# Kernel optimization log

Hardware: AMD Instinct MI355X
Metric: run time of the kernel (lower is better)

## Reference

```python
import jax, jax.numpy as jnp
import numpy as np
from jax import lax

DIM = 1024      # model dim
DS = 16         # d_state
DC = 4          # d_conv
EXP = 2
DI = DIM * EXP  # d_inner = 2048
B, L = 2, 1024


def setup_inputs() -> dict:
    key = jax.random.key(0)
    ks = jax.random.split(key, 10)
    s = lambda k, shape, sc: jax.random.normal(k, shape, jnp.float32) * sc
    return {
        "x": s(ks[0], (B, L, DIM), 1.0),
        "norm_w": jnp.ones((DIM,), jnp.float32),
        "norm_b": jnp.zeros((DIM,), jnp.float32),
        "in_proj_w": s(ks[1], (2 * DI, DIM), DIM ** -0.5),
        "conv_w": s(ks[2], (DI, 1, DC), DC ** -0.5),   # depthwise: (out=DI, in/groups=1, K)
        "conv_b": jnp.zeros((DI,), jnp.float32),
        "x_proj_w": s(ks[3], (2 * DS + 1, DI), DI ** -0.5),
        "dt_w": s(ks[4], (DI, 1), 1.0),
        "dt_b": jax.random.uniform(ks[5], (DI,), jnp.float32, -0.001, 0.001),
        "A_log": s(ks[6], (DI, DS), 1.0),              # self.A (randn); A = -exp(A_log)
        "D_skip": jnp.ones((DI,), jnp.float32),
        "out_proj_w": s(ks[7], (DIM, DI), DI ** -0.5),
    }


def _ssm(x, x_proj_w, dt_w, dt_b, A_log, D_skip):
    # x: (B, L, DI)
    xp = jnp.einsum('bli,pi->blp', x, x_proj_w)            # (B, L, 2*DS+1)
    delta = jax.nn.softplus(xp[..., :1] * dt_w[:, 0] + dt_b)  # (B, L, DI)
    Bp = xp[..., 1:DS + 1]                                  # (B, L, DS)
    Cp = xp[..., DS + 1:]                                   # (B, L, DS)
    A = -jnp.exp(A_log)                                     # (DI, DS)
    dA = jnp.exp(delta[..., None] * A)                      # (B, L, DI, DS)
    dB = delta[..., None] * Bp[:, :, None, :] * x[..., None]  # (B, L, DI, DS)

    def step(h, inp):
        dA_t, dB_t, C_t = inp                               # (B,DI,DS),(B,DI,DS),(B,DS)
        h = dA_t * h + dB_t
        return h, jnp.einsum('bdn,bn->bd', h, C_t)

    h0 = jnp.zeros((x.shape[0], DI, DS), x.dtype)
    _, ys = lax.scan(step, h0, (jnp.swapaxes(dA, 0, 1),
                                jnp.swapaxes(dB, 0, 1),
                                jnp.swapaxes(Cp, 0, 1)))
    y = jnp.swapaxes(ys, 0, 1)                              # (B, L, DI)
    return y + x * D_skip


def reference(x, norm_w, norm_b, in_proj_w, conv_w, conv_b,
              x_proj_w, dt_w, dt_b, A_log, D_skip, out_proj_w):
    # LayerNorm
    mu = x.mean(-1, keepdims=True)
    var = ((x - mu) ** 2).mean(-1, keepdims=True)
    xn = (x - mu) * lax.rsqrt(var + 1e-5) * norm_w + norm_b
    # input projection and gate split
    xz = jnp.einsum('bld,pd->blp', xn, in_proj_w)           # (B, L, 2*DI)
    xi, z = xz[..., :DI], xz[..., DI:]
    # causal depthwise conv (torch pads K-1 both sides then slices [:L] == left-pad K-1)
    xc = lax.conv_general_dilated(jnp.swapaxes(xi, 1, 2), conv_w, (1,),
                                  [(DC - 1, 0)], feature_group_count=DI,
                                  dimension_numbers=('NCH', 'OIH', 'NCH'))
    xc = jnp.swapaxes(xc + conv_b[None, :, None], 1, 2)     # (B, L, DI)
    xc = jax.nn.silu(xc)
    y = _ssm(xc, x_proj_w, dt_w, dt_b, A_log, D_skip)
    y = y * jax.nn.silu(z)
    return x + jnp.einsum('bli,di->bld', y, out_proj_w)
```

## Files before the change

kernel.cpp:

```cpp
#include <hip/hip_runtime.h>
#include <stdint.h>

#define BATCH 2
#define SEQ   1024
#define DIM_  1024
#define DS_   16
#define DI_   2048
#define NTOK  (BATCH*SEQ)
#define NSEG  32
#define LSEG  (SEQ/NSEG)

typedef unsigned short u16;
using s16x8 = __attribute__((ext_vector_type(8))) short;
using f32x4 = __attribute__((ext_vector_type(4))) float;
using u16x4 = __attribute__((ext_vector_type(4))) unsigned short;
using u16x8 = __attribute__((ext_vector_type(8))) unsigned short;

__device__ __forceinline__ float bf2f(u16 u) {
  union { unsigned int i; float f; } c; c.i = ((unsigned int)u) << 16; return c.f;
}
__device__ __forceinline__ u16 f2bf(float f) {
  union { float f; unsigned int i; } c; c.f = f;
  unsigned int r = c.i + 0x7fffu + ((c.i >> 16) & 1u);
  return (u16)(r >> 16);
}
__device__ __forceinline__ float softplus_f(float x) {
  return (x > 15.f) ? x : __logf(1.f + __expf(x));
}

__global__ __launch_bounds__(256) void cvt_kernel(const float* __restrict__ a,
    u16* __restrict__ o, int n4) {
  int i = blockIdx.x * 256 + threadIdx.x;
  if (i >= n4) return;
  float4 v = ((const float4*)a)[i];
  u16x4 r; r[0] = f2bf(v.x); r[1] = f2bf(v.y); r[2] = f2bf(v.z); r[3] = f2bf(v.w);
  ((u16x4*)o)[i] = r;
}

__global__ __launch_bounds__(256) void cvt_pad_kernel(const float* __restrict__ a,
    u16* __restrict__ o) {
  int i = blockIdx.x * 256 + threadIdx.x;
  if (i >= 32768) return;
  int p = (i * 4) >> 11;
  u16x4 r;
  if (p < 33) {
    float4 v = ((const float4*)a)[i];
    r[0] = f2bf(v.x); r[1] = f2bf(v.y); r[2] = f2bf(v.z); r[3] = f2bf(v.w);
  } else {
    r[0] = 0; r[1] = 0; r[2] = 0; r[3] = 0;
  }
  ((u16x4*)o)[i] = r;
}

__global__ __launch_bounds__(256) void ln_kernel(const float* __restrict__ x,
    const float* __restrict__ w, const float* __restrict__ b, u16* __restrict__ xn) {
  int t = blockIdx.x, tid = threadIdx.x;
  const float* row = x + (size_t)t * DIM_;
  float4 v = ((const float4*)row)[tid];
  float f[4] = {v.x, v.y, v.z, v.w};
  float s = 0.f, sq = 0.f;
#pragma unroll
  for (int j = 0; j < 4; j++) { s += f[j]; sq += f[j] * f[j]; }
#pragma unroll
  for (int m = 1; m < 64; m <<= 1) { s += __shfl_xor(s, m); sq += __shfl_xor(sq, m); }
  __shared__ float rs_[4], rq_[4];
  int wv = tid >> 6;
  if ((tid & 63) == 0) { rs_[wv] = s; rq_[wv] = sq; }
  __syncthreads();
  s = rs_[0] + rs_[1] + rs_[2] + rs_[3];
  sq = rq_[0] + rq_[1] + rq_[2] + rq_[3];
  float mu = s * (1.0f / DIM_);
  float var = sq * (1.0f / DIM_) - mu * mu;
  float rstd = rsqrtf(var + 1e-5f);
  float4 wn = ((const float4*)w)[tid];
  float4 bn = ((const float4*)b)[tid];
  u16x4 o;
  o[0] = f2bf((f[0] - mu) * rstd * wn.x + bn.x);
  o[1] = f2bf((f[1] - mu) * rstd * wn.y + bn.y);
  o[2] = f2bf((f[2] - mu) * rstd * wn.z + bn.z);
  o[3] = f2bf((f[3] - mu) * rstd * wn.w + bn.w);
  *(u16x4*)(xn + (size_t)t * DIM_ + tid * 4) = o;
}

template<int TBM, int TBN, int BK, typename OUT, int EPI, int KSPLIT = 1, int SWZ = 0>
__global__ __launch_bounds__(256) void gemm_bt(const u16* __restrict__ A,
    const u16* __restrict__ Wt, OUT* __restrict__ C, const float* __restrict__ X,
    int M, int N, int K) {
  constexpr int LDT = BK + 8;
  constexpr int TPR = BK / 8;
  constexpr int RPP = 256 / TPR;
  constexpr int ALn = TBM / RPP;
  constexpr int BLn = TBN / RPP;
  constexpr int KK = BK / 32;
  constexpr int WM = TBM / 2, WN = TBN / 2;
  constexpr int MI = WM / 16, NJ = WN / 16;
  __shared__ __align__(16) u16 sA[TBM * LDT];
  __shared__ __align__(16) u16 sB[TBN * LDT];
  const int tid = threadIdx.x;
  const int lane = tid & 63, wv = tid >> 6;
  const int wm = (wv >> 1) * WM, wn = (wv & 1) * WN;
  const int bxl = SWZ ? ((blockIdx.x & 7) * (gridDim.x >> 3) + (blockIdx.x >> 3))
                      : blockIdx.x;
  const int bm0 = blockIdx.y * TBM, bn0 = bxl * TBN;
  const int q = lane >> 4, r16 = lane & 15;
  const int srow = tid / TPR, scol = (tid % TPR) * 8;
  const int kc = K / KSPLIT;
  const int k0 = (KSPLIT > 1) ? blockIdx.z * kc : 0;
  const int kend = k0 + kc;

  f32x4 acc[MI][NJ];
#pragma unroll
  for (int i = 0; i < MI; i++)
#pragma unroll
    for (int j = 0; j < NJ; j++)
#pragma unroll
      for (int r = 0; r < 4; r++) acc[i][j][r] = 0.f;

  const u16* Ag = A + (size_t)bm0 * K + scol + k0;
  const u16* Wg = Wt + (size_t)bn0 * K + scol + k0;
  s16x8 ra[ALn], rb[BLn];
#pragma unroll
  for (int i = 0; i < ALn; i++) ra[i] = *(const s16x8*)(Ag + (size_t)(srow + i * RPP) * K);
#pragma unroll
  for (int i = 0; i < BLn; i++) rb[i] = *(const s16x8*)(Wg + (size_t)(srow + i * RPP) * K);

  for (int kt = k0; kt < kend; kt += BK) {
    __syncthreads();
#pragma unroll
    for (int i = 0; i < ALn; i++) *(s16x8*)&sA[(srow + i * RPP) * LDT + scol] = ra[i];
#pragma unroll
    for (int i = 0; i < BLn; i++) *(s16x8*)&sB[(srow + i * RPP) * LDT + scol] = rb[i];
    __syncthreads();
    int kn = kt + BK - k0;
    if (kn < kc) {
#pragma unroll
      for (int i = 0; i < ALn; i++) ra[i] = *(const s16x8*)(Ag + (size_t)(srow + i * RPP) * K + kn);
#pragma unroll
      for (int i = 0; i < BLn; i++) rb[i] = *(const s16x8*)(Wg + (size_t)(srow + i * RPP) * K + kn);
    }
#pragma unroll
    for (int kk = 0; kk < KK; kk++) {
      s16x8 fa[MI], fb[NJ];
#pragma unroll
      for (int i = 0; i < MI; i++)
        fa[i] = *(const s16x8*)&sA[(wm + i * 16 + r16) * LDT + kk * 32 + q * 8];
#pragma unroll
      for (int j = 0; j < NJ; j++)
        fb[j] = *(const s16x8*)&sB[(wn + j * 16 + r16) * LDT + kk * 32 + q * 8];
#pragma unroll
      for (int i = 0; i < MI; i++)
#pragma unroll
        for (int j = 0; j < NJ; j++)
          acc[i][j] = __builtin_amdgcn_mfma_f32_16x16x32_bf16(fa[i], fb[j], acc[i][j], 0, 0, 0);
    }
  }
  OUT* Cz = C + ((KSPLIT > 1) ? (size_t)blockIdx.z * M * N : 0);
#pragma unroll
  for (int i = 0; i < MI; i++)
#pragma unroll
    for (int j = 0; j < NJ; j++) {
      int row0 = bm0 + wm + i * 16 + q * 4;
      int col = bn0 + wn + j * 16 + r16;
#pragma unroll
      for (int r = 0; r < 4; r++) {
        size_t off = (size_t)(row0 + r) * N + col;
        float v = acc[i][j][r];
        if constexpr (EPI == 1) v += X[off];
        if constexpr (sizeof(OUT) == 2) Cz[off] = f2bf(v);
        else                            Cz[off] = v;
      }
    }
}

__global__ __launch_bounds__(256) void reduce_out_kernel(const float* __restrict__ part,
    const float* __restrict__ x, float* __restrict__ out) {
  int g = blockIdx.x * 256 + threadIdx.x;
  constexpr size_t STR = (size_t)NTOK * DIM_ / 4;
  float4 a = ((const float4*)part)[g];
  float4 b = ((const float4*)part)[g + STR];
  float4 xv = ((const float4*)x)[g];
  float4 o;
  o.x = xv.x + a.x + b.x;
  o.y = xv.y + a.y + b.y;
  o.z = xv.z + a.z + b.z;
  o.w = xv.w + a.w + b.w;
  ((float4*)out)[g] = o;
}

__global__ __launch_bounds__(256) void conv_silu_kernel(const u16* __restrict__ xz,
    const float* __restrict__ cw, const float* __restrict__ cb, u16* __restrict__ xc) {
  int t = blockIdx.x;
  int l = t & (SEQ - 1);
  int c0 = threadIdx.x * 8;
  float acc[8], wk[8][4];
#pragma unroll
  for (int j = 0; j < 8; j++) {
    float4 wv = ((const float4*)cw)[c0 + j];
    wk[j][0] = wv.x; wk[j][1] = wv.y; wk[j][2] = wv.z; wk[j][3] = wv.w;
    acc[j] = cb[c0 + j];
  }
#pragma unroll
  for (int k = 0; k < 4; k++) {
    int lk = l - 3 + k;
    if (lk >= 0) {
      u16x8 v = *(const u16x8*)(xz + (size_t)(t - 3 + k) * (2 * DI_) + c0);
#pragma unroll
      for (int j = 0; j < 8; j++) acc[j] = fmaf(bf2f(v[j]), wk[j][k], acc[j]);
    }
  }
  u16x8 o;
#pragma unroll
  for (int j = 0; j < 8; j++) {
    float a = acc[j];
    o[j] = f2bf(a / (1.0f + __expf(-a)));
  }
  *(u16x8*)(xc + (size_t)t * DI_ + c0) = o;
}

__global__ __launch_bounds__(256) void xp_finish_kernel(const float* __restrict__ part,
    const float* __restrict__ dtw, const float* __restrict__ dtb,
    u16* __restrict__ xz, float* __restrict__ bc) {
  int t = blockIdx.x;
  int tid = threadIdx.x;
  __shared__ float xps[64];
  if (tid < 64) {
    float s = 0.f;
#pragma unroll
    for (int k = 0; k < 8; k++)
      s += part[(size_t)k * NTOK * 64 + (size_t)t * 64 + tid];
    xps[tid] = s;
  }
  __syncthreads();
  if (tid < 32) bc[(size_t)t * 32 + tid] = xps[1 + tid];
  float dr = xps[0];
  int c0 = tid * 8;
  float wv[8], bv[8];
  *(float4*)wv = ((const float4*)(dtw + c0))[0];
  *(float4*)(wv + 4) = ((const float4*)(dtw + c0))[1];
  *(float4*)bv = ((const float4*)(dtb + c0))[0];
  *(float4*)(bv + 4) = ((const float4*)(dtb + c0))[1];
  u16x8 o;
#pragma unroll
  for (int j = 0; j < 8; j++) o[j] = f2bf(softplus_f(dr * wv[j] + bv[j]));
  *(u16x8*)(xz + (size_t)t * (2 * DI_) + c0) = o;
}

__global__ __launch_bounds__(256) void scan_pass1(const float* __restrict__ bc,
    const u16* __restrict__ dlt, const u16* __restrict__ xc,
    const float* __restrict__ A_log, float* __restrict__ P, float* __restrict__ Q) {
  int tid = threadIdx.x;
  int lane = tid & 63, wv = tid >> 6;
  int nl = (lane & 3) * 4;
  int d = blockIdx.x * 64 + wv * 16 + (lane >> 2);
  int s = blockIdx.y, b = blockIdx.z;
  int t0 = b * SEQ + s * LSEG;
  float4 Ain = *(const float4*)(A_log + d * DS_ + nl);
  f32x4 Av;
  Av[0] = -__expf(Ain.x); Av[1] = -__expf(Ain.y);
  Av[2] = -__expf(Ain.z); Av[3] = -__expf(Ain.w);
  f32x4 Pv, h;
#pragma unroll
  for (int i = 0; i < 4; i++) { Pv[i] = 1.f; h[i] = 0.f; }
#pragma unroll 4
  for (int j = 0; j < LSEG; j++) {
    int t = t0 + j;
    float delta = bf2f(dlt[(size_t)t * (2 * DI_) + d]);
    float xcv = bf2f(xc[(size_t)t * DI_ + d]);
    float4 B4 = *(const float4*)(bc + (size_t)t * 32 + nl);
    float du = delta * xcv;
#pragma unroll
    for (int i = 0; i < 4; i++) {
      float a = __expf(delta * Av[i]);
      Pv[i] *= a;
      float bi = (i == 0) ? B4.x : (i == 1) ? B4.y : (i == 2) ? B4.z : B4.w;
      h[i] = fmaf(a, h[i], du * bi);
    }
  }
  size_t idx = ((size_t)((b * NSEG + s) * DI_ + d)) * 16 + nl;
  *(f32x4*)(P + idx) = Pv;
  *(f32x4*)(Q + idx) = h;
}

__global__ __launch_bounds__(256) void scan_combine(const float* __restrict__ P,
    float* __restrict__ Q) {
  int g = blockIdx.x * 256 + threadIdx.x;
  int n = g & 15, d = (g >> 4) & (DI_ - 1), b = g >> 15;
  size_t base = ((size_t)b * NSEG * DI_ + d) * 16 + n;
  constexpr size_t STR = (size_t)DI_ * 16;
  float p_[NSEG], q_[NSEG];
#pragma unroll
  for (int s = 0; s < NSEG; s++) {
    p_[s] = P[base + s * STR];
    q_[s] = Q[base + s * STR];
  }
  float hh = 0.f;
#pragma unroll
  for (int s = 0; s < NSEG; s++) {
    Q[base + s * STR] = hh;
    hh = fmaf(p_[s], hh, q_[s]);
  }
}

__global__ __launch_bounds__(256) void scan_pass2(const float* __restrict__ bc,
    const u16* __restrict__ dlt, const u16* __restrict__ xc,
    const float* __restrict__ A_log, const float* __restrict__ Dskip,
    const float* __restrict__ Hin, u16* __restrict__ yb) {
  int tid = threadIdx.x;
  int lane = tid & 63, wv = tid >> 6;
  int nl = (lane & 3) * 4;
  int d = blockIdx.x * 64 + wv * 16 + (lane >> 2);
  int s = blockIdx.y, b = blockIdx.z;
  int t0 = b * SEQ + s * LSEG;
  float4 Ain = *(const float4*)(A_log + d * DS_ + nl);
  f32x4 Av;
  Av[0] = -__expf(Ain.x); Av[1] = -__expf(Ain.y);
  Av[2] = -__expf(Ain.z); Av[3] = -__expf(Ain.w);
  float Dv = Dskip[d];
  size_t idx = ((size_t)((b * NSEG + s) * DI_ + d)) * 16 + nl;
  f32x4 h = *(const f32x4*)(Hin + idx);
#pragma unroll 4
  for (int j = 0; j < LSEG; j++) {
    int t = t0 + j;
    float delta = bf2f(dlt[(size_t)t * (2 * DI_) + d]);
    float xcv = bf2f(xc[(size_t)t * DI_ + d]);
    float4 B4 = *(const float4*)(bc + (size_t)t * 32 + nl);
    float4 C4 = *(const float4*)(bc + (size_t)t * 32 + 16 + nl);
    float du = delta * xcv;
#pragma unroll
    for (int i = 0; i < 4; i++) {
      float a = __expf(delta * Av[i]);
      float bi = (i == 0) ? B4.x : (i == 1) ? B4.y : (i == 2) ? B4.z : B4.w;
      h[i] = fmaf(a, h[i], du * bi);
    }
    float p = h[0] * C4.x;
    p = fmaf(h[1], C4.y, p);
    p = fmaf(h[2], C4.z, p);
    p = fmaf(h[3], C4.w, p);
    p += __shfl_xor(p, 1);
    p += __shfl_xor(p, 2);
    if ((lane & 3) == 0) {
      float z = bf2f(dlt[(size_t)t * (2 * DI_) + DI_ + d]);
      float sz = z / (1.0f + __expf(-z));
      yb[(size_t)t * DI_ + d] = f2bf((p + xcv * Dv) * sz);
    }
  }
}

extern "C" void kernel_launch(void* const* d_in, const int* in_sizes, int n_in,
                              void* d_out, int out_size, void* d_ws, size_t ws_size,
                              hipStream_t stream) {
  const float* x      = (const float*)d_in[0];
  const float* norm_w = (const float*)d_in[1];
  const float* norm_b = (const float*)d_in[2];
  const float* in_w   = (const float*)d_in[3];
  const float* conv_w = (const float*)d_in[4];
  const float* conv_b = (const float*)d_in[5];
  const float* xproj_w= (const float*)d_in[6];
  const float* dt_w   = (const float*)d_in[7];
  const float* dt_b   = (const float*)d_in[8];
  const float* A_log  = (const float*)d_in[9];
  const float* D_skip = (const float*)d_in[10];
  const float* out_w  = (const float*)d_in[11];
  float* out = (float*)d_out;

  char* ws = (char*)d_ws;
  size_t off = 0;
  auto alloc = [&](size_t bytes) { void* p = ws + off; off += (bytes + 255) & ~255ULL; return p; };
  u16* xpw_bf = (u16*)alloc((size_t)64 * DI_ * 2);
  u16* xz     = (u16*)alloc((size_t)NTOK * 2 * DI_ * 2);
  u16* xc     = (u16*)alloc((size_t)NTOK * DI_ * 2);
  float* bc   = (float*)alloc((size_t)NTOK * 32 * 4);
  char* regionA = (char*)alloc((size_t)BATCH * NSEG * DI_ * 16 * 4);
  float* Q = (float*)alloc((size_t)BATCH * NSEG * DI_ * 16 * 4);
  u16* xn   = (u16*)regionA;
  float* P  = (float*)regionA;
  u16* yb   = (u16*)regionA;
  u16* in_w_bf  = (u16*)Q;
  float* xp_part = Q;
  u16* out_w_bf = (u16*)Q;
  float* out_part = (float*)xz;

  cvt_kernel<<<(2 * DI_ * DIM_ / 4 + 255) / 256, 256, 0, stream>>>(in_w, in_w_bf,
                                                                   2 * DI_ * DIM_ / 4);
  cvt_pad_kernel<<<128, 256, 0, stream>>>(xproj_w, xpw_bf);
  ln_kernel<<<NTOK, 256, 0, stream>>>(x, norm_w, norm_b, xn);
  gemm_bt<128, 128, 64, u16, 0, 1, 1><<<dim3((2 * DI_) / 128, NTOK / 128), 256, 0, stream>>>(
      xn, in_w_bf, xz, nullptr, NTOK, 2 * DI_, DIM_);
  conv_silu_kernel<<<NTOK, 256, 0, stream>>>(xz, conv_w, conv_b, xc);
  gemm_bt<64, 64, 32, float, 0, 8><<<dim3(1, NTOK / 64, 8), 256, 0, stream>>>(
      xc, xpw_bf, xp_part, nullptr, NTOK, 64, DI_);
  xp_finish_kernel<<<NTOK, 256, 0, stream>>>(xp_part, dt_w, dt_b, xz, bc);
  scan_pass1<<<dim3(DI_ / 64, NSEG, BATCH), 256, 0, stream>>>(bc, xz, xc, A_log, P, Q);
  scan_combine<<<BATCH * DI_ * 16 / 256, 256, 0, stream>>>(P, Q);
  scan_pass2<<<dim3(DI_ / 64, NSEG, BATCH), 256, 0, stream>>>(bc, xz, xc, A_log, D_skip,
                                                              Q, yb);
  cvt_kernel<<<(DIM_ * DI_ / 4 + 255) / 256, 256, 0, stream>>>(out_w, out_w_bf,
                                                               DIM_ * DI_ / 4);
  gemm_bt<128, 64, 64, float, 0, 2, 1><<<dim3(DIM_ / 64, NTOK / 128, 2), 256, 0, stream>>>(
      yb, out_w_bf, out_part, nullptr, NTOK, DIM_, DI_);
  reduce_out_kernel<<<NTOK * DIM_ / 4 / 256, 256, 0, stream>>>(out_part, x, out);
}
```

Measured before the change: 241.7 us.

## Merge weight conversions, fuse residual into out-proj GEMM, unroll scans deeper

Folds the three weight-conversion launches into a single kernel and gives every buffer its own workspace region, where before several shared aliased memory. The split-K out-projection GEMM with its separate reduce kernel becomes a single 64x64-tile GEMM with a residual-add epilogue. Both scan passes unroll their time loops by 8 instead of 4. This removes launches and the partial-sum round trip through memory, at the cost of fewer output tiles for the 2048-long reduction and a larger workspace.

```diff
diff --git a/kernel.cpp b/kernel.cpp
--- a/kernel.cpp
+++ b/kernel.cpp
@@ -27,29 +27,31 @@
 __device__ __forceinline__ float softplus_f(float x) {
   return (x > 15.f) ? x : __logf(1.f + __expf(x));
 }
-
-__global__ __launch_bounds__(256) void cvt_kernel(const float* __restrict__ a,
-    u16* __restrict__ o, int n4) {
+__device__ __forceinline__ u16x4 f4_to_bf(float4 v) {
+  u16x4 r; r[0] = f2bf(v.x); r[1] = f2bf(v.y); r[2] = f2bf(v.z); r[3] = f2bf(v.w);
+  return r;
+}
+
+#define N4_INW  (2 * DI_ * DIM_ / 4)
+#define N4_OUTW (DIM_ * DI_ / 4)
+__global__ __launch_bounds__(256) void cvt_all_kernel(const float* __restrict__ in_w,
+    const float* __restrict__ out_w, const float* __restrict__ xproj_w,
+    u16* __restrict__ in_w_bf, u16* __restrict__ out_w_bf, u16* __restrict__ xpw_bf) {
   int i = blockIdx.x * 256 + threadIdx.x;
-  if (i >= n4) return;
-  float4 v = ((const float4*)a)[i];
-  u16x4 r; r[0] = f2bf(v.x); r[1] = f2bf(v.y); r[2] = f2bf(v.z); r[3] = f2bf(v.w);
-  ((u16x4*)o)[i] = r;
-}
-
-__global__ __launch_bounds__(256) void cvt_pad_kernel(const float* __restrict__ a,
-    u16* __restrict__ o) {
-  int i = blockIdx.x * 256 + threadIdx.x;
-  if (i >= 32768) return;
-  int p = (i * 4) >> 11;
-  u16x4 r;
-  if (p < 33) {
-    float4 v = ((const float4*)a)[i];
-    r[0] = f2bf(v.x); r[1] = f2bf(v.y); r[2] = f2bf(v.z); r[3] = f2bf(v.w);
+  if (i < N4_INW) {
+    ((u16x4*)in_w_bf)[i] = f4_to_bf(((const float4*)in_w)[i]);
+  } else if (i < N4_INW + N4_OUTW) {
+    int j = i - N4_INW;
+    ((u16x4*)out_w_bf)[j] = f4_to_bf(((const float4*)out_w)[j]);
   } else {
-    r[0] = 0; r[1] = 0; r[2] = 0; r[3] = 0;
-  }
-  ((u16x4*)o)[i] = r;
+    int j = i - (N4_INW + N4_OUTW);
+    if (j >= 32768) return;
+    int p = (j * 4) >> 11;
+    u16x4 r;
+    if (p < 33) r = f4_to_bf(((const float4*)xproj_w)[j]);
+    else { r[0] = 0; r[1] = 0; r[2] = 0; r[3] = 0; }
+    ((u16x4*)xpw_bf)[j] = r;
+  }
 }
 
 __global__ __launch_bounds__(256) void ln_kernel(const float* __restrict__ x,
@@ -172,21 +174,6 @@
     }
 }
 
-__global__ __launch_bounds__(256) void reduce_out_kernel(const float* __restrict__ part,
-    const float* __restrict__ x, float* __restrict__ out) {
-  int g = blockIdx.x * 256 + threadIdx.x;
-  constexpr size_t STR = (size_t)NTOK * DIM_ / 4;
-  float4 a = ((const float4*)part)[g];
-  float4 b = ((const float4*)part)[g + STR];
-  float4 xv = ((const float4*)x)[g];
-  float4 o;
-  o.x = xv.x + a.x + b.x;
-  o.y = xv.y + a.y + b.y;
-  o.z = xv.z + a.z + b.z;
-  o.w = xv.w + a.w + b.w;
-  ((float4*)out)[g] = o;
-}
-
 __global__ __launch_bounds__(256) void conv_silu_kernel(const u16* __restrict__ xz,
     const float* __restrict__ cw, const float* __restrict__ cb, u16* __restrict__ xc) {
   int t = blockIdx.x;
@@ -261,7 +248,7 @@
   f32x4 Pv, h;
 #pragma unroll
   for (int i = 0; i < 4; i++) { Pv[i] = 1.f; h[i] = 0.f; }
-#pragma unroll 4
+#pragma unroll 8
   for (int j = 0; j < LSEG; j++) {
     int t = t0 + j;
     float delta = bf2f(dlt[(size_t)t * (2 * DI_) + d]);
@@ -318,7 +305,7 @@
   float Dv = Dskip[d];
   size_t idx = ((size_t)((b * NSEG + s) * DI_ + d)) * 16 + nl;
   f32x4 h = *(const f32x4*)(Hin + idx);
-#pragma unroll 4
+#pragma unroll 8
   for (int j = 0; j < LSEG; j++) {
     int t = t0 + j;
     float delta = bf2f(dlt[(size_t)t * (2 * DI_) + d]);
@@ -366,23 +353,20 @@
   char* ws = (char*)d_ws;
   size_t off = 0;
   auto alloc = [&](size_t bytes) { void* p = ws + off; off += (bytes + 255) & ~255ULL; return p; };
-  u16* xpw_bf = (u16*)alloc((size_t)64 * DI_ * 2);
-  u16* xz     = (u16*)alloc((size_t)NTOK * 2 * DI_ * 2);
-  u16* xc     = (u16*)alloc((size_t)NTOK * DI_ * 2);
-  float* bc   = (float*)alloc((size_t)NTOK * 32 * 4);
-  char* regionA = (char*)alloc((size_t)BATCH * NSEG * DI_ * 16 * 4);
-  float* Q = (float*)alloc((size_t)BATCH * NSEG * DI_ * 16 * 4);
-  u16* xn   = (u16*)regionA;
-  float* P  = (float*)regionA;
-  u16* yb   = (u16*)regionA;
-  u16* in_w_bf  = (u16*)Q;
-  float* xp_part = Q;
-  u16* out_w_bf = (u16*)Q;
-  float* out_part = (float*)xz;
-
-  cvt_kernel<<<(2 * DI_ * DIM_ / 4 + 255) / 256, 256, 0, stream>>>(in_w, in_w_bf,
-                                                                   2 * DI_ * DIM_ / 4);
-  cvt_pad_kernel<<<128, 256, 0, stream>>>(xproj_w, xpw_bf);
+  u16* in_w_bf  = (u16*)alloc((size_t)2 * DI_ * DIM_ * 2);
+  u16* out_w_bf = (u16*)alloc((size_t)DIM_ * DI_ * 2);
+  u16* xpw_bf   = (u16*)alloc((size_t)64 * DI_ * 2);
+  u16* xn       = (u16*)alloc((size_t)NTOK * DIM_ * 2);
+  u16* xz       = (u16*)alloc((size_t)NTOK * 2 * DI_ * 2);
+  u16* xc       = (u16*)alloc((size_t)NTOK * DI_ * 2);
+  float* bc     = (float*)alloc((size_t)NTOK * 32 * 4);
+  float* xp_part= (float*)alloc((size_t)8 * NTOK * 64 * 4);
+  float* P      = (float*)alloc((size_t)BATCH * NSEG * DI_ * 16 * 4);
+  float* Q      = (float*)alloc((size_t)BATCH * NSEG * DI_ * 16 * 4);
+  u16* yb       = (u16*)alloc((size_t)NTOK * DI_ * 2);
+
+  cvt_all_kernel<<<(N4_INW + N4_OUTW + 32768 + 255) / 256, 256, 0, stream>>>(
+      in_w, out_w, xproj_w, in_w_bf, out_w_bf, xpw_bf);
   ln_kernel<<<NTOK, 256, 0, stream>>>(x, norm_w, norm_b, xn);
   gemm_bt<128, 128, 64, u16, 0, 1, 1><<<dim3((2 * DI_) / 128, NTOK / 128), 256, 0, stream>>>(
       xn, in_w_bf, xz, nullptr, NTOK, 2 * DI_, DIM_);
@@ -394,9 +378,6 @@
   scan_combine<<<BATCH * DI_ * 16 / 256, 256, 0, stream>>>(P, Q);
   scan_pass2<<<dim3(DI_ / 64, NSEG, BATCH), 256, 0, stream>>>(bc, xz, xc, A_log, D_skip,
                                                               Q, yb);
-  cvt_kernel<<<(DIM_ * DI_ / 4 + 255) / 256, 256, 0, stream>>>(out_w, out_w_bf,
-                                                               DIM_ * DI_ / 4);
-  gemm_bt<128, 64, 64, float, 0, 2, 1><<<dim3(DIM_ / 64, NTOK / 128, 2), 256, 0, stream>>>(
-      yb, out_w_bf, out_part, nullptr, NTOK, DIM_, DI_);
-  reduce_out_kernel<<<NTOK * DIM_ / 4 / 256, 256, 0, stream>>>(out_part, x, out);
-}
+  gemm_bt<64, 64, 64, float, 1, 1, 1><<<dim3(DIM_ / 64, NTOK / 64), 256, 0, stream>>>(
+      yb, out_w_bf, out, x, NTOK, DIM_, DI_);
+}
```

Result: faster. 235.5 us (-2.6%).
